# Kernel optimization log

Measured on AMD Instinct MI355X. Metric: run time of the kernel, lower is better.

The kernel has to match this reference:

```python
import jax, jax.numpy as jnp
import numpy as np
from jax import lax

IN_CH = 512
OUT_CH = 512
HEAD_DIM = 8
NUM_HEADS = IN_CH // HEAD_DIM  # 64
INNER = NUM_HEADS * HEAD_DIM   # 512
KSIZE = 5
EPS = 1e-15
BN_EPS = 1e-5
DN = ('NCHW', 'OIHW', 'NCHW')


def setup_inputs() -> dict:
    key = jax.random.key(0)
    ks = jax.random.split(key, 10)
    s = 0.02
    return {
        'hidden_states': jax.random.normal(ks[0], (4, IN_CH, 64, 64), jnp.float32),
        'wq': jax.random.normal(ks[1], (INNER, IN_CH), jnp.float32) * s,
        'wk': jax.random.normal(ks[2], (INNER, IN_CH), jnp.float32) * s,
        'wv': jax.random.normal(ks[3], (INNER, IN_CH), jnp.float32) * s,
        # depthwise conv: groups = 3*INNER, 1 in-channel per group
        'dw_kernel': jax.random.normal(ks[4], (3 * INNER, 1, KSIZE, KSIZE), jnp.float32) * s,
        # grouped 1x1 conv: groups = 3*NUM_HEADS -> 3*INNER/(3*NUM_HEADS)=HEAD_DIM in-ch/group
        'pw_kernel': jax.random.normal(ks[5], (3 * INNER, HEAD_DIM, 1, 1), jnp.float32) * s,
        # proj_out 1x1: in = INNER*(1+len(kernel_sizes)) = 2*INNER
        'proj_kernel': jax.random.normal(ks[6], (OUT_CH, 2 * INNER, 1, 1), jnp.float32) * s,
        'bn_gamma': jnp.ones((OUT_CH,), jnp.float32),
        'bn_beta': jnp.zeros((OUT_CH,), jnp.float32),
        'bn_mean': jnp.zeros((OUT_CH,), jnp.float32),
        'bn_var': jnp.ones((OUT_CH,), jnp.float32),
    }


def _forward(hidden_states, wq, wk, wv, dw_kernel, pw_kernel, proj_kernel,
             bn_gamma, bn_beta, bn_mean, bn_var):
    x = hidden_states  # [B,C,H,W]
    B, _, H, W = x.shape
    h = jnp.moveaxis(x, 1, -1)  # [B,H,W,C]
    q = h @ wq.T
    k = h @ wk.T
    v = h @ wv.T
    qkv = jnp.moveaxis(jnp.concatenate([q, k, v], axis=-1), -1, 1)  # [B,3*INNER,H,W]

    # multi-scale aggregation: depthwise 5x5 then grouped 1x1
    dw = lax.conv_general_dilated(qkv, dw_kernel, (1, 1), 'SAME',
                                  feature_group_count=3 * INNER, dimension_numbers=DN)
    pw = lax.conv_general_dilated(dw, pw_kernel, (1, 1), 'VALID',
                                  feature_group_count=3 * NUM_HEADS, dimension_numbers=DN)
    qkv_all = jnp.concatenate([qkv, pw], axis=1)  # [B, 2*3*INNER, H, W]

    # relu linear attention (fp32)
    N = H * W
    d = HEAD_DIM
    f = qkv_all.astype(jnp.float32).reshape(B, -1, 3 * d, N)  # [B, nh_total, 3d, N]
    query = jax.nn.relu(f[:, :, :d])
    key_ = jax.nn.relu(f[:, :, d:2 * d])
    value = f[:, :, 2 * d:]
    value_pad = jnp.concatenate([value, jnp.ones_like(value[:, :, :1])], axis=2)  # [B,nh,d+1,N]
    scores = jnp.einsum('bhdn,bhen->bhde', value_pad, key_)   # [B,nh,d+1,d]
    out = jnp.einsum('bhde,bhen->bhdn', scores, query)         # [B,nh,d+1,N]
    out = out[:, :, :-1] / (out[:, :, -1:] + EPS)
    out = out.reshape(B, -1, H, W).astype(qkv_all.dtype)        # [B, 2*INNER, H, W]

    # proj_out 1x1 conv + BatchNorm2d (eval mode, running stats)
    y = lax.conv_general_dilated(out, proj_kernel, (1, 1), 'VALID', dimension_numbers=DN)
    inv = bn_gamma / jnp.sqrt(bn_var + BN_EPS)
    y = y * inv[None, :, None, None] + (bn_beta - bn_mean * inv)[None, :, None, None]
    return y + x


def reference(hidden_states, wq, wk, wv, dw_kernel, pw_kernel, proj_kernel,
              bn_gamma, bn_beta, bn_mean, bn_var):
    return _forward(hidden_states, wq, wk, wv, dw_kernel, pw_kernel, proj_kernel,
                    bn_gamma, bn_beta, bn_mean, bn_var)
```

## Files before the change

kernel.cpp:

```cpp
#include <hip/hip_runtime.h>
#include <hip/hip_bf16.h>

typedef __hip_bfloat16 bf16;
typedef __attribute__((ext_vector_type(8))) short bf16x8;
typedef __attribute__((ext_vector_type(4))) float f32x4;

#define BATCH 4
#define CIN   512
#define HW    64
#define NPIX  4096
#define CALL  3072
#define NHEAD 128
#define EPS_LITE 1e-15f
#define BN_EPS   1e-5f


__device__ __forceinline__ short f2bf(float f) {
    __hip_bfloat16 h = __float2bfloat16(f);
    short s; __builtin_memcpy(&s, &h, 2); return s;
}
__device__ __forceinline__ float bfl(unsigned u) {
    unsigned v = u << 16; float f; __builtin_memcpy(&f, &v, 4); return f;
}
__device__ __forceinline__ float bfh(unsigned u) {
    unsigned v = u & 0xffff0000u; float f; __builtin_memcpy(&f, &v, 4); return f;
}
__device__ __forceinline__ unsigned packbf(float a, float b) {
    return (unsigned)(unsigned short)f2bf(a) | ((unsigned)(unsigned short)f2bf(b) << 16);
}
__device__ __forceinline__ void gll16(const void* gsrc, void* ldst) {
    __builtin_amdgcn_global_load_lds(
        (const __attribute__((address_space(1))) unsigned int*)gsrc,
        (__attribute__((address_space(3))) unsigned int*)ldst, 16, 0, 0);
}

__global__ __launch_bounds__(256) void k_cvtw(const float* __restrict__ wq,
                                              const float* __restrict__ wk,
                                              const float* __restrict__ wv,
                                              const float* __restrict__ pj,
                                              bf16* __restrict__ Wbf,
                                              bf16* __restrict__ Pbf) {
    const int e = (blockIdx.x * 256 + threadIdx.x) * 4;
    const float* s; bf16* dst;
    if (e < 786432) {
        int o;
        if (e < 262144)      { s = wq; o = e; }
        else if (e < 524288) { s = wk; o = e - 262144; }
        else                 { s = wv; o = e - 524288; }
        f32x4 v = *(const f32x4*)(s + o);
        dst = Wbf + e;
        *(ushort2*)dst = make_ushort2((unsigned short)f2bf(v[0]), (unsigned short)f2bf(v[1]));
        *(ushort2*)(dst + 2) = make_ushort2((unsigned short)f2bf(v[2]), (unsigned short)f2bf(v[3]));
    } else {
        const int o = e - 786432;
        f32x4 v = *(const f32x4*)(pj + o);
        dst = Pbf + o;
        *(ushort2*)dst = make_ushort2((unsigned short)f2bf(v[0]), (unsigned short)f2bf(v[1]));
        *(ushort2*)(dst + 2) = make_ushort2((unsigned short)f2bf(v[2]), (unsigned short)f2bf(v[3]));
    }
}

__global__ __launch_bounds__(256) void k_cvtx(const float* __restrict__ x,
                                              bf16* __restrict__ xT) {
    __shared__ short lds[64][72];
    const int t   = threadIdx.x;
    const int px0 = blockIdx.x * 64;
    const int k0  = blockIdx.y * 64;
    const int b   = blockIdx.z;

    const int pr = t & 15, rr = t >> 4;
#pragma unroll
    for (int it = 0; it < 4; ++it) {
        const int row = it * 16 + rr;
        f32x4 v = *(const f32x4*)(x + (size_t)(b * CIN + k0 + row) * NPIX + px0 + pr * 4);
#pragma unroll
        for (int i = 0; i < 4; ++i) lds[pr * 4 + i][row] = f2bf(v[i]);
    }
    __syncthreads();

    const int px = t >> 2, kc = t & 3;
    uint4 u0 = *(const uint4*)&lds[px][kc * 16];
    uint4 u1 = *(const uint4*)&lds[px][kc * 16 + 8];
    bf16* dst = xT + ((size_t)b * NPIX + px0 + px) * 512 + k0 + kc * 16;
    *(uint4*)dst = u0;
    *(uint4*)(dst + 8) = u1;
}

template<int KD, int MT, bool PROJ>
__global__ __launch_bounds__(256) void k_gemm3(
        const bf16* __restrict__ Xt,
        const bf16* __restrict__ Wb,
        bf16* __restrict__ Obf,
        const float* __restrict__ gm, const float* __restrict__ bt,
        const float* __restrict__ mu, const float* __restrict__ va,
        const float* __restrict__ resid, float* __restrict__ Of)
{
    constexpr int NT = KD / 32;
    constexpr int MS = MT / 32;
    constexpr int AG = MT / 64;
    __shared__ short Ald[2][MT * 32];
    __shared__ short Bld[2][128 * 32];

    const int t    = threadIdx.x;
    const int lane = t & 63;
    const int w    = t >> 6;
    const int wm   = w >> 1, wn = w & 1;
    const int n0   = blockIdx.x * 128;
    const int c0   = blockIdx.y * MT;
    const int b    = blockIdx.z;

    const bf16* abase = Wb + (size_t)(c0 + w * (MT / 4) + (lane >> 2)) * KD + (lane & 3) * 8;
    const bf16* bbase = Xt + ((size_t)b * NPIX + n0 + w * 32 + (lane >> 2)) * KD + (lane & 3) * 8;

    auto stage = [&](int s, int buf) {
#pragma unroll
        for (int q = 0; q < AG; ++q)
            gll16(abase + (size_t)q * 16 * KD + s * 32,
                  &Ald[buf][(w * (MT / 4) + q * 16) * 32]);
#pragma unroll
        for (int q = 0; q < 2; ++q)
            gll16(bbase + (size_t)q * 16 * KD + s * 32,
                  &Bld[buf][(w * 32 + q * 16) * 32]);
    };

    f32x4 acc[MS][4];
#pragma unroll
    for (int ms = 0; ms < MS; ++ms)
#pragma unroll
        for (int ns = 0; ns < 4; ++ns)
#pragma unroll
            for (int j = 0; j < 4; ++j) acc[ms][ns][j] = 0.f;

    stage(0, 0);
    __syncthreads();

    const int l15 = lane & 15, l4 = lane >> 4;
    for (int s = 0; s < NT; ++s) {
        const int cur = s & 1;
        if (s + 1 < NT) stage(s + 1, cur ^ 1);

        bf16x8 af[MS], bv[4];
#pragma unroll
        for (int ms = 0; ms < MS; ++ms)
            af[ms] = *(const bf16x8*)&Ald[cur][(wm * (MT / 2) + ms * 16 + l15) * 32 + l4 * 8];
#pragma unroll
        for (int ns = 0; ns < 4; ++ns)
            bv[ns] = *(const bf16x8*)&Bld[cur][(wn * 64 + ns * 16 + l15) * 32 + l4 * 8];
#pragma unroll
        for (int ms = 0; ms < MS; ++ms)
#pragma unroll
            for (int ns = 0; ns < 4; ++ns)
                acc[ms][ns] = __builtin_amdgcn_mfma_f32_16x16x32_bf16(
                    af[ms], bv[ns], acc[ms][ns], 0, 0, 0);

        __syncthreads();
    }

    if (!PROJ) {
#pragma unroll
        for (int ms = 0; ms < MS; ++ms) {
            const int crow = c0 + wm * (MT / 2) + ms * 16 + l4 * 4;
#pragma unroll
            for (int ns = 0; ns < 4; ++ns) {
                const int ncol = n0 + wn * 64 + ns * 16 + l15;
#pragma unroll
                for (int j = 0; j < 4; ++j) {
                    bf16 h; short sv = f2bf(acc[ms][ns][j]);
                    __builtin_memcpy(&h, &sv, 2);
                    Obf[((size_t)b * CALL + crow + j) * NPIX + ncol] = h;
                }
            }
        }
    } else {
#pragma unroll
        for (int ms = 0; ms < MS; ++ms) {
            const int crow = c0 + wm * (MT / 2) + ms * 16 + l4 * 4;
#pragma unroll
            for (int j = 0; j < 4; ++j) {
                const int o = crow + j;
                const float inv = gm[o] / sqrtf(va[o] + BN_EPS);
                const float sh  = bt[o] - mu[o] * inv;
#pragma unroll
                for (int ns = 0; ns < 4; ++ns) {
                    const int ncol = n0 + wn * 64 + ns * 16 + l15;
                    const size_t idx = ((size_t)b * 512 + o) * NPIX + ncol;
                    Of[idx] = acc[ms][ns][j] * inv + sh + resid[idx];
                }
            }
        }
    }
}

__global__ __launch_bounds__(256) void k_dwpw(const float* __restrict__ dwk,
                                              const float* __restrict__ pwk,
                                              bf16* __restrict__ qkv_all) {
    __shared__ short in_lds[8 * 20 * 80];
    __shared__ short dw_lds[8 * 16 * 64];

    const int t  = threadIdx.x;
    const int g  = blockIdx.y;
    const int b  = blockIdx.z;
    const int y0 = blockIdx.x * 16;

    const bf16* src = qkv_all + ((size_t)b * CALL + g * 8) * NPIX;
#pragma unroll
    for (int i = 0; i < 7; ++i) {
        const int v = i * 256 + t;
        if (v < 1600) {
            const int ch  = v / 200;
            const int rem = v % 200;
            const int row = rem / 10;
            const int seg = rem % 10;
            const int grow = y0 + row - 2;
            uint4 val = make_uint4(0u, 0u, 0u, 0u);
            if (seg >= 1 && seg <= 8 && grow >= 0 && grow < HW)
                val = *(const uint4*)(src + (size_t)ch * NPIX + grow * HW + (seg - 1) * 8);
            *(uint4*)&in_lds[ch * 1600 + row * 80 + seg * 8] = val;
        }
    }

    const int lane = t & 63;
    const int w    = t >> 6;
    const int xb   = lane & 7;
    const int ch   = lane >> 3;
    const int x0   = xb * 8;

    float kc[25];
    {
        const float* kp = dwk + (size_t)(g * 8 + ch) * 25;
#pragma unroll
        for (int i = 0; i < 25; ++i) kc[i] = kp[i];
    }
    __syncthreads();

    float A[5][12];
    const short* cb = &in_lds[ch * 1600 + x0];

    auto loadrow = [&](int L, float* f) {
        const short* rp = cb + L * 80;
        uint2 lo = *(const uint2*)(rp + 4);
        uint4 md = *(const uint4*)(rp + 8);
        uint2 hi = *(const uint2*)(rp + 16);
        f[0]  = bfl(lo.y); f[1]  = bfh(lo.y);
        f[2]  = bfl(md.x); f[3]  = bfh(md.x);
        f[4]  = bfl(md.y); f[5]  = bfh(md.y);
        f[6]  = bfl(md.z); f[7]  = bfh(md.z);
        f[8]  = bfl(md.w); f[9]  = bfh(md.w);
        f[10] = bfl(hi.x); f[11] = bfh(hi.x);
    };

    const int r0 = w * 4;
    loadrow(r0 + 0, A[0]);
    loadrow(r0 + 1, A[1]);
    loadrow(r0 + 2, A[2]);
    loadrow(r0 + 3, A[3]);

#pragma unroll
    for (int ri = 0; ri < 4; ++ri) {
        loadrow(r0 + ri + 4, A[(ri + 4) % 5]);
        float acc[8];
#pragma unroll
        for (int i = 0; i < 8; ++i) acc[i] = 0.f;
#pragma unroll
        for (int dy = 0; dy < 5; ++dy) {
            const float* Ar = A[(ri + dy) % 5];
#pragma unroll
            for (int dx = 0; dx < 5; ++dx) {
                const float kv = kc[dy * 5 + dx];
#pragma unroll
                for (int i = 0; i < 8; ++i)
                    acc[i] += Ar[i + dx] * kv;
            }
        }
        uint4 pk;
        pk.x = packbf(acc[0], acc[1]);
        pk.y = packbf(acc[2], acc[3]);
        pk.z = packbf(acc[4], acc[5]);
        pk.w = packbf(acc[6], acc[7]);
        *(uint4*)&dw_lds[ch * 1024 + (r0 + ri) * 64 + x0] = pk;
    }
    __syncthreads();

    const float* pwb = pwk + (size_t)g * 64;
#pragma unroll
    for (int it = 0; it < 2; ++it) {
        const int p2 = (it * 256 + t) * 2;
        float v0[8], v1[8];
#pragma unroll
        for (int ci = 0; ci < 8; ++ci) {
            const unsigned u = *(const unsigned*)&dw_lds[ci * 1024 + p2];
            v0[ci] = bfl(u); v1[ci] = bfh(u);
        }
        bf16* op = qkv_all + ((size_t)b * CALL + 1536 + g * 8) * NPIX + y0 * HW + p2;
#pragma unroll
        for (int o = 0; o < 8; ++o) {
            float s0 = 0.f, s1 = 0.f;
#pragma unroll
            for (int ci = 0; ci < 8; ++ci) {
                const float wv = pwb[o * 8 + ci];
                s0 += wv * v0[ci]; s1 += wv * v1[ci];
            }
            *(unsigned*)(op + (size_t)o * NPIX) = packbf(s0, s1);
        }
    }
}

__global__ __launch_bounds__(64) void k_scores(const bf16* __restrict__ qkv_all,
                                               float* __restrict__ part) {
    const int lane = threadIdx.x;
    const int h = blockIdx.y;
    const int b = blockIdx.z;
    const bf16* base = qkv_all + ((size_t)b * CALL + h * 24) * NPIX;

    float acc[72];
#pragma unroll
    for (int i = 0; i < 72; ++i) acc[i] = 0.f;

    for (int it = 0; it < 4; ++it) {
        const int n = blockIdx.x * 512 + it * 128 + lane * 2;
        const bf16* p = base + n;
        float k0[8], k1[8], v0[8], v1[8];
#pragma unroll
        for (int e = 0; e < 8; ++e) {
            const unsigned u = *(const unsigned*)&p[(size_t)(8 + e) * NPIX];
            k0[e] = fmaxf(bfl(u), 0.f); k1[e] = fmaxf(bfh(u), 0.f);
        }
#pragma unroll
        for (int d = 0; d < 8; ++d) {
            const unsigned u = *(const unsigned*)&p[(size_t)(16 + d) * NPIX];
            v0[d] = bfl(u); v1[d] = bfh(u);
        }
#pragma unroll
        for (int d = 0; d < 9; ++d) {
            const float vd0 = (d < 8) ? v0[d] : 1.f;
            const float vd1 = (d < 8) ? v1[d] : 1.f;
#pragma unroll
            for (int e = 0; e < 8; ++e)
                acc[d * 8 + e] += vd0 * k0[e] + vd1 * k1[e];
        }
    }

    const int bh = b * NHEAD + h;
#pragma unroll
    for (int i = 0; i < 72; ++i) {
        float v = acc[i];
        for (int off = 32; off; off >>= 1) v += __shfl_xor(v, off, 64);
        if (lane == 0) part[((size_t)bh * 72 + i) * 8 + blockIdx.x] = v;
    }
}

__global__ __launch_bounds__(128) void k_scores2(const float* __restrict__ part,
                                                 float* __restrict__ scores) {
    const int bh = blockIdx.x;
    const int i = threadIdx.x;
    if (i < 72) {
        float s = 0.f;
#pragma unroll
        for (int ns = 0; ns < 8; ++ns) s += part[((size_t)bh * 72 + i) * 8 + ns];
        scores[(size_t)bh * 72 + i] = s;
    }
}

__global__ __launch_bounds__(256) void k_att3(const bf16* __restrict__ qkv_all,
                                              const float* __restrict__ scores,
                                              bf16* __restrict__ attT) {
    const int px = blockIdx.x * 256 + threadIdx.x;
    const int h = blockIdx.y;
    const int b = blockIdx.z;

    const bf16* qb = qkv_all + ((size_t)b * CALL + h * 24) * NPIX + px;
    float q[8];
#pragma unroll
    for (int e = 0; e < 8; ++e)
        q[e] = fmaxf(__bfloat162float(qb[(size_t)e * NPIX]), 0.f);

    const float* sp = scores + (size_t)(b * NHEAD + h) * 72;
    float num[9];
#pragma unroll
    for (int d = 0; d < 9; ++d) {
        float s = 0.f;
#pragma unroll
        for (int e = 0; e < 8; ++e) s += sp[d * 8 + e] * q[e];
        num[d] = s;
    }
    const float inv = 1.f / (num[8] + EPS_LITE);
    uint4 pk;
    pk.x = packbf(num[0] * inv, num[1] * inv);
    pk.y = packbf(num[2] * inv, num[3] * inv);
    pk.z = packbf(num[4] * inv, num[5] * inv);
    pk.w = packbf(num[6] * inv, num[7] * inv);
    *(uint4*)(attT + ((size_t)b * NPIX + px) * 1024 + h * 8) = pk;
}

extern "C" void kernel_launch(void* const* d_in, const int* in_sizes, int n_in,
                              void* d_out, int out_size, void* d_ws, size_t ws_size,
                              hipStream_t stream) {
    const float* x   = (const float*)d_in[0];
    const float* wq  = (const float*)d_in[1];
    const float* wk  = (const float*)d_in[2];
    const float* wv  = (const float*)d_in[3];
    const float* dwk = (const float*)d_in[4];
    const float* pwk = (const float*)d_in[5];
    const float* pj  = (const float*)d_in[6];
    const float* gm  = (const float*)d_in[7];
    const float* bt  = (const float*)d_in[8];
    const float* mu  = (const float*)d_in[9];
    const float* va  = (const float*)d_in[10];
    float* out = (float*)d_out;

    char* ws = (char*)d_ws;
    bf16*  qkv_all = (bf16*)(ws);
    bf16*  attT    = (bf16*)(ws + 100663296);
    bf16*  xT      = (bf16*)(ws + 100663296);
    float* part    = (float*)(ws + 134217728);
    float* scores  = (float*)(ws + 135397376);
    bf16*  Wbf     = (bf16*)(ws + 135544832);
    bf16*  Pbf     = (bf16*)(ws + 137117696);

    k_cvtw<<<dim3(1280), 256, 0, stream>>>(wq, wk, wv, pj, Wbf, Pbf);
    k_cvtx<<<dim3(64, 8, BATCH), 256, 0, stream>>>(x, xT);
    k_gemm3<512, 128, false><<<dim3(32, 12, BATCH), 256, 0, stream>>>(
        xT, Wbf, qkv_all, nullptr, nullptr, nullptr, nullptr, nullptr, nullptr);
    k_dwpw   <<<dim3( 4, 192, BATCH), 256, 0, stream>>>(dwk, pwk, qkv_all);
    k_scores <<<dim3( 8, 128, BATCH),  64, 0, stream>>>(qkv_all, part);
    k_scores2<<<dim3(512), 128, 0, stream>>>(part, scores);
    k_att3   <<<dim3(16, 128, BATCH), 256, 0, stream>>>(qkv_all, scores, attT);
    k_gemm3<1024, 64, true><<<dim3(32, 8, BATCH), 256, 0, stream>>>(
        attT, Pbf, nullptr, gm, bt, mu, va, x, out);
}
```

Measured before the change: 174.8 us.

## Fuse score reduction into attention kernel and double dwpw row tile

The separate k_scores2 launch is dropped. Each k_att3 block now reduces the 8 partial score sums for its head into shared memory before applying them, which removes one kernel launch and the scores round-trip. The fused version repeats that small reduction in each of the 16 pixel blocks per head. Separately, k_dwpw now processes 32 rows per block with 512 threads instead of 16 rows with 256, which lowers the halo reload overhead from 20/16 to 36/32 rows. In exchange it uses more LDS per block and launches half as many blocks.

Measured after the change: 182.6 us. 1.04x slower.

```diff
diff --git a/kernel.cpp b/kernel.cpp
--- a/kernel.cpp
+++ b/kernel.cpp
@@ -191,31 +191,33 @@
     }
 }
 
-__global__ __launch_bounds__(256) void k_dwpw(const float* __restrict__ dwk,
+#define DW_ICS (36 * 80)
+#define DW_DCS (32 * 64)
+__global__ __launch_bounds__(512) void k_dwpw(const float* __restrict__ dwk,
                                               const float* __restrict__ pwk,
                                               bf16* __restrict__ qkv_all) {
-    __shared__ short in_lds[8 * 20 * 80];
-    __shared__ short dw_lds[8 * 16 * 64];
+    __shared__ short in_lds[8 * DW_ICS];
+    __shared__ short dw_lds[8 * DW_DCS];
 
     const int t  = threadIdx.x;
     const int g  = blockIdx.y;
     const int b  = blockIdx.z;
-    const int y0 = blockIdx.x * 16;
+    const int y0 = blockIdx.x * 32;
 
     const bf16* src = qkv_all + ((size_t)b * CALL + g * 8) * NPIX;
 #pragma unroll
-    for (int i = 0; i < 7; ++i) {
-        const int v = i * 256 + t;
-        if (v < 1600) {
-            const int ch  = v / 200;
-            const int rem = v % 200;
+    for (int i = 0; i < 6; ++i) {
+        const int v = i * 512 + t;
+        if (v < 2880) {
+            const int ch  = v / 360;
+            const int rem = v % 360;
             const int row = rem / 10;
             const int seg = rem % 10;
             const int grow = y0 + row - 2;
             uint4 val = make_uint4(0u, 0u, 0u, 0u);
             if (seg >= 1 && seg <= 8 && grow >= 0 && grow < HW)
                 val = *(const uint4*)(src + (size_t)ch * NPIX + grow * HW + (seg - 1) * 8);
-            *(uint4*)&in_lds[ch * 1600 + row * 80 + seg * 8] = val;
+            *(uint4*)&in_lds[ch * DW_ICS + row * 80 + seg * 8] = val;
         }
     }
 
@@ -234,7 +236,7 @@
     __syncthreads();
 
     float A[5][12];
-    const short* cb = &in_lds[ch * 1600 + x0];
+    const short* cb = &in_lds[ch * DW_ICS + x0];
 
     auto loadrow = [&](int L, float* f) {
         const short* rp = cb + L * 80;
@@ -277,18 +279,18 @@
         pk.y = packbf(acc[2], acc[3]);
         pk.z = packbf(acc[4], acc[5]);
         pk.w = packbf(acc[6], acc[7]);
-        *(uint4*)&dw_lds[ch * 1024 + (r0 + ri) * 64 + x0] = pk;
+        *(uint4*)&dw_lds[ch * DW_DCS + (r0 + ri) * 64 + x0] = pk;
     }
     __syncthreads();
 
     const float* pwb = pwk + (size_t)g * 64;
 #pragma unroll
     for (int it = 0; it < 2; ++it) {
-        const int p2 = (it * 256 + t) * 2;
+        const int p2 = (it * 512 + t) * 2;
         float v0[8], v1[8];
 #pragma unroll
         for (int ci = 0; ci < 8; ++ci) {
-            const unsigned u = *(const unsigned*)&dw_lds[ci * 1024 + p2];
+            const unsigned u = *(const unsigned*)&dw_lds[ci * DW_DCS + p2];
             v0[ci] = bfl(u); v1[ci] = bfh(u);
         }
         bf16* op = qkv_all + ((size_t)b * CALL + 1536 + g * 8) * NPIX + y0 * HW + p2;
@@ -349,38 +351,36 @@
     }
 }
 
-__global__ __launch_bounds__(128) void k_scores2(const float* __restrict__ part,
-                                                 float* __restrict__ scores) {
-    const int bh = blockIdx.x;
-    const int i = threadIdx.x;
-    if (i < 72) {
+__global__ __launch_bounds__(256) void k_att3(const bf16* __restrict__ qkv_all,
+                                              const float* __restrict__ part,
+                                              bf16* __restrict__ attT) {
+    __shared__ float sc[72];
+    const int t  = threadIdx.x;
+    const int h  = blockIdx.y;
+    const int b  = blockIdx.z;
+    const int bh = b * NHEAD + h;
+
+    if (t < 72) {
         float s = 0.f;
 #pragma unroll
-        for (int ns = 0; ns < 8; ++ns) s += part[((size_t)bh * 72 + i) * 8 + ns];
-        scores[(size_t)bh * 72 + i] = s;
-    }
-}
-
-__global__ __launch_bounds__(256) void k_att3(const bf16* __restrict__ qkv_all,
-                                              const float* __restrict__ scores,
-                                              bf16* __restrict__ attT) {
-    const int px = blockIdx.x * 256 + threadIdx.x;
-    const int h = blockIdx.y;
-    const int b = blockIdx.z;
-
+        for (int ns = 0; ns < 8; ++ns) s += part[((size_t)bh * 72 + t) * 8 + ns];
+        sc[t] = s;
+    }
+    __syncthreads();
+
+    const int px = blockIdx.x * 256 + t;
     const bf16* qb = qkv_all + ((size_t)b * CALL + h * 24) * NPIX + px;
     float q[8];
 #pragma unroll
     for (int e = 0; e < 8; ++e)
         q[e] = fmaxf(__bfloat162float(qb[(size_t)e * NPIX]), 0.f);
 
-    const float* sp = scores + (size_t)(b * NHEAD + h) * 72;
     float num[9];
 #pragma unroll
     for (int d = 0; d < 9; ++d) {
         float s = 0.f;
 #pragma unroll
-        for (int e = 0; e < 8; ++e) s += sp[d * 8 + e] * q[e];
+        for (int e = 0; e < 8; ++e) s += sc[d * 8 + e] * q[e];
         num[d] = s;
     }
     const float inv = 1.f / (num[8] + EPS_LITE);
@@ -413,7 +413,6 @@
     bf16*  attT    = (bf16*)(ws + 100663296);
     bf16*  xT      = (bf16*)(ws + 100663296);
     float* part    = (float*)(ws + 134217728);
-    float* scores  = (float*)(ws + 135397376);
     bf16*  Wbf     = (bf16*)(ws + 135544832);
     bf16*  Pbf     = (bf16*)(ws + 137117696);
 
@@ -421,10 +420,9 @@
     k_cvtx<<<dim3(64, 8, BATCH), 256, 0, stream>>>(x, xT);
     k_gemm3<512, 128, false><<<dim3(32, 12, BATCH), 256, 0, stream>>>(
         xT, Wbf, qkv_all, nullptr, nullptr, nullptr, nullptr, nullptr, nullptr);
-    k_dwpw   <<<dim3( 4, 192, BATCH), 256, 0, stream>>>(dwk, pwk, qkv_all);
-    k_scores <<<dim3( 8, 128, BATCH),  64, 0, stream>>>(qkv_all, part);
-    k_scores2<<<dim3(512), 128, 0, stream>>>(part, scores);
-    k_att3   <<<dim3(16, 128, BATCH), 256, 0, stream>>>(qkv_all, scores, attT);
+    k_dwpw  <<<dim3( 2, 192, BATCH), 512, 0, stream>>>(dwk, pwk, qkv_all);
+    k_scores<<<dim3( 8, 128, BATCH),  64, 0, stream>>>(qkv_all, part);
+    k_att3  <<<dim3(16, 128, BATCH), 256, 0, stream>>>(qkv_all, part, attT);
     k_gemm3<1024, 64, true><<<dim3(32, 8, BATCH), 256, 0, stream>>>(
         attT, Pbf, nullptr, gm, bt, mu, va, x, out);
 }
```
